# Optimization experiments

Hardware: AMD Instinct MI355X
Metric: run time of the kernel (lower is better)

The kernel has to match this reference:

```python
import jax, jax.numpy as jnp
import numpy as np

NUM_HEADS = 6


def setup_inputs() -> dict:
    key = jax.random.key(0)
    k1, k2, k3 = jax.random.split(key, 3)
    b_, n, c = 512, 256, 192
    nw = 64
    x = jax.random.normal(k1, (b_, n, c), dtype=jnp.float32)
    mask = jnp.zeros((nw, n, n), dtype=jnp.float32)  # 0 / -inf additive window mask
    W_qkv = jax.random.normal(k2, (3 * c, c), dtype=jnp.float32) * 0.02
    W_proj = jax.random.normal(k3, (c, c), dtype=jnp.float32) * 0.02
    b_proj = jnp.zeros((c,), dtype=jnp.float32)
    return {"x": x, "mask": mask, "W_qkv": W_qkv, "W_proj": W_proj, "b_proj": b_proj}


def reference(x, mask, W_qkv, W_proj, b_proj):
    b_, n, c = x.shape
    h = NUM_HEADS
    d = c // h
    scale = d ** (-0.5)
    # qkv projection (no bias): (b_, n, 3, h, d) -> (3, b_, h, n, d)
    qkv = (x @ W_qkv.T).reshape(b_, n, 3, h, d).transpose(2, 0, 3, 1, 4)
    q, k, v = qkv[0], qkv[1], qkv[2]
    q = q * scale
    attn = jnp.einsum('bhid,bhjd->bhij', q, k)  # (b_, h, n, n)
    nw = mask.shape[0]
    # add per-window mask bias: view as (B, nw, h, n, n) + (1, nw, 1, n, n)
    attn = attn.reshape(b_ // nw, nw, h, n, n) + mask[None, :, None, :, :]
    attn = attn.reshape(b_, h, n, n)
    attn = jax.nn.softmax(attn, axis=-1)
    out = jnp.einsum('bhij,bhjd->bhid', attn, v)  # (b_, h, n, d)
    out = out.transpose(0, 2, 1, 3).reshape(b_, n, c)
    return out @ W_proj.T + b_proj
```

## Files before the change

### kernel.cpp

```cpp
#include <hip/hip_runtime.h>
#include <hip/hip_bf16.h>
#include <stdint.h>

typedef short bf16x8 __attribute__((ext_vector_type(8)));
typedef float f32x4 __attribute__((ext_vector_type(4)));

#define B_   512
#define N_   256
#define C_   192
#define H_   6
#define D_   32
#define NW_  64

__device__ __forceinline__ uint16_t f2bf(float f) {
    uint32_t u = __builtin_bit_cast(uint32_t, f);
    u += 0x7FFFu + ((u >> 16) & 1u);
    return (uint16_t)(u >> 16);
}

__device__ __forceinline__ uint32_t pk_bf16(float a, float b) {
    float2 t; t.x = a; t.y = b;
    __hip_bfloat162 h = __float22bfloat162_rn(t);
    uint32_t u;
    __builtin_memcpy(&u, &h, 4);
    return u;
}

__device__ __forceinline__ bf16x8 ld_bf8(const uint16_t* p) {
    uint4 u = *reinterpret_cast<const uint4*>(p);
    return __builtin_bit_cast(bf16x8, u);
}

__global__ void prep_kernel(const float* __restrict__ mask,
                            const float* __restrict__ wqkv,
                            const float* __restrict__ wproj,
                            uint16_t* __restrict__ sel,
                            uint16_t* __restrict__ wqkv_bf,
                            uint16_t* __restrict__ wproj_bf,
                            unsigned* __restrict__ flag) {
    const int64_t NSEL = (int64_t)NW_ * N_ * N_;
    const int64_t NWQ  = 3 * C_ * C_;
    const int64_t NWP  = (int64_t)C_ * C_;
    int64_t i = (int64_t)blockIdx.x * blockDim.x + threadIdx.x;
    int64_t stride = (int64_t)gridDim.x * blockDim.x;
    bool nz = false;
    for (; i < NSEL + NWQ + NWP; i += stride) {
        if (i < NSEL) {
            float m = mask[i];
            nz |= (m != 0.0f);
            sel[i] = (m == 0.0f) ? 0xFFFFu : 0u;
        } else if (i < NSEL + NWQ) {
            int64_t j = i - NSEL;
            wqkv_bf[j] = f2bf(wqkv[j]);
        } else {
            int64_t j = i - NSEL - NWQ;
            wproj_bf[j] = f2bf(wproj[j]);
        }
    }
    if (flag && __any(nz) && ((threadIdx.x & 63) == 0))
        atomicOr(flag, 1u);
}

#define SA 200
#define SB 72
__global__ __launch_bounds__(512, 4)
void qkv_kernel(const float* __restrict__ x, const uint16_t* __restrict__ wq,
                uint16_t* __restrict__ qbuf, uint16_t* __restrict__ kbuf,
                uint16_t* __restrict__ vtbuf) {
    __shared__ __align__(16) uint16_t Alds[128 * SA];
    __shared__ __align__(16) uint16_t Blds[192 * SB];
    const int tid  = threadIdx.x;
    const int lane = tid & 63;
    const int wv   = tid >> 6;
    const int wrow = wv >> 2;
    const int wcol = wv & 3;
    const int quad = lane >> 4;
    const int l15  = lane & 15;
    const int m0   = blockIdx.x * 128;

#pragma unroll
    for (int p = 0; p < 12; p++) {
        int f = p * 512 + tid;
        int row = f / 48, c4 = f % 48;
        const float4 v = *reinterpret_cast<const float4*>(
            x + (int64_t)(m0 + row) * 192 + c4 * 4);
        uint2 d;
        d.x = pk_bf16(v.x, v.y);
        d.y = pk_bf16(v.z, v.w);
        *reinterpret_cast<uint2*>(&Alds[row * SA + c4 * 4]) = d;
    }

    const float scale = 0.17677669529663687f * 1.4426950408889634f;

    for (int cb = 0; cb < 3; cb++) {
        f32x4 acc[4][3];
#pragma unroll
        for (int i = 0; i < 4; i++)
#pragma unroll
            for (int j = 0; j < 3; j++) acc[i][j] = (f32x4)0.f;

        for (int k0 = 0; k0 < 192; k0 += 64) {
            __syncthreads();
#pragma unroll
            for (int p = 0; p < 3; p++) {
                int u = p * 512 + tid;
                int row = u >> 3, c8 = u & 7;
                uint4 w = *reinterpret_cast<const uint4*>(
                    wq + (int64_t)(cb * 192 + row) * 192 + k0 + c8 * 8);
                *reinterpret_cast<uint4*>(&Blds[row * SB + c8 * 8]) = w;
            }
            __syncthreads();
#pragma unroll
            for (int ks = 0; ks < 2; ks++) {
                bf16x8 xf[4], wf[3];
#pragma unroll
                for (int i = 0; i < 4; i++)
                    xf[i] = *reinterpret_cast<const bf16x8*>(
                        &Alds[(wrow * 64 + i * 16 + l15) * SA + k0 + ks * 32 + quad * 8]);
#pragma unroll
                for (int j = 0; j < 3; j++)
                    wf[j] = *reinterpret_cast<const bf16x8*>(
                        &Blds[(wcol * 48 + j * 16 + l15) * SB + ks * 32 + quad * 8]);
                if (cb < 2) {
#pragma unroll
                    for (int i = 0; i < 4; i++)
#pragma unroll
                        for (int j = 0; j < 3; j++)
                            acc[i][j] = __builtin_amdgcn_mfma_f32_16x16x32_bf16(
                                wf[j], xf[i], acc[i][j], 0, 0, 0);
                } else {
#pragma unroll
                    for (int i = 0; i < 4; i++)
#pragma unroll
                        for (int j = 0; j < 3; j++)
                            acc[i][j] = __builtin_amdgcn_mfma_f32_16x16x32_bf16(
                                xf[i], wf[j], acc[i][j], 0, 0, 0);
                }
            }
        }

        if (cb < 2) {
            uint16_t* dst = (cb == 0) ? qbuf : kbuf;
            const float sc = (cb == 0) ? scale : 1.0f;
#pragma unroll
            for (int i = 0; i < 4; i++) {
                int m = m0 + wrow * 64 + i * 16 + l15;
                int b = m >> 8, pos = m & 255;
#pragma unroll
                for (int j = 0; j < 3; j++) {
                    int cbase = wcol * 48 + j * 16 + quad * 4;
                    int h = cbase >> 5, d0 = cbase & 31;
                    int64_t bh = (int64_t)b * H_ + h;
                    uint2 s;
                    s.x = pk_bf16(acc[i][j][0] * sc, acc[i][j][1] * sc);
                    s.y = pk_bf16(acc[i][j][2] * sc, acc[i][j][3] * sc);
                    *reinterpret_cast<uint2*>(&dst[(bh * N_ + pos) * D_ + d0]) = s;
                }
            }
        } else {
#pragma unroll
            for (int i = 0; i < 4; i++) {
                int m = m0 + wrow * 64 + i * 16 + quad * 4;
                int b = m >> 8, pos0 = m & 255;
#pragma unroll
                for (int j = 0; j < 3; j++) {
                    int c = wcol * 48 + j * 16 + l15;
                    int h = c >> 5, d = c & 31;
                    int64_t bh = (int64_t)b * H_ + h;
                    uint2 s;
                    s.x = pk_bf16(acc[i][j][0], acc[i][j][1]);
                    s.y = pk_bf16(acc[i][j][2], acc[i][j][3]);
                    *reinterpret_cast<uint2*>(&vtbuf[(bh * D_ + d) * N_ + pos0]) = s;
                }
            }
        }
    }
}

__global__ __launch_bounds__(256, 3)
void attn_kernel(const uint16_t* __restrict__ qbuf, const uint16_t* __restrict__ kbuf,
                 const uint16_t* __restrict__ vtbuf, const uint16_t* __restrict__ sel,
                 const unsigned* __restrict__ flag,
                 uint16_t* __restrict__ aout) {
    __shared__ __align__(16) uint16_t Plds[4 * 2 * 32 * 40];
    const int bi = blockIdx.x;
    const int h  = bi % 6;
    const int r_ = bi / 6;
    const int ih = r_ & 1;
    const int g  = (r_ >> 1) & 7;
    const int w  = r_ >> 4;
    const int b  = g * 64 + w;
    const int tid  = threadIdx.x;
    const int lane = tid & 63;
    const int wv   = tid >> 6;
    const int quad = lane >> 4;
    const int l15  = lane & 15;
    const int i0   = ih * 128 + wv * 32;
    const bool hasmask = flag ? (*flag != 0u) : true;
    const int64_t bh = (int64_t)b * H_ + h;
    const uint16_t* qB = qbuf  + bh * N_ * D_;
    const uint16_t* kB = kbuf  + bh * N_ * D_;
    const uint16_t* vB = vtbuf + bh * D_ * N_;
    const uint16_t* sB = sel   + (int64_t)w * N_ * N_;
    uint16_t* Pw = &Plds[wv * 2 * 32 * 40];

    bf16x8 qf[2];
#pragma unroll
    for (int it = 0; it < 2; it++)
        qf[it] = ld_bf8(&qB[(i0 + it * 16 + l15) * D_ + quad * 8]);

    f32x4 oacc[2][2];
    f32x4 lacc[2];
#pragma unroll
    for (int mt = 0; mt < 2; mt++) {
        oacc[mt][0] = (f32x4)0.f; oacc[mt][1] = (f32x4)0.f; lacc[mt] = (f32x4)0.f;
    }
    bf16x8 ones;
#pragma unroll
    for (int e = 0; e < 8; e++) ones[e] = (short)0x3F80;

    bf16x8 kf[4];
#pragma unroll
    for (int jt = 0; jt < 4; jt++)
        kf[jt] = ld_bf8(&kB[(jt * 16 + l15) * D_ + quad * 8]);

    for (int jc = 0; jc < 4; jc++) {
        const int j0 = jc * 64;

        bf16x8 kfn[4];
        if (jc < 3) {
#pragma unroll
            for (int jt = 0; jt < 4; jt++)
                kfn[jt] = ld_bf8(&kB[(j0 + 64 + jt * 16 + l15) * D_ + quad * 8]);
        }

        bf16x8 vf[2][2];
#pragma unroll
        for (int hf = 0; hf < 2; hf++)
#pragma unroll
            for (int nt = 0; nt < 2; nt++)
                vf[hf][nt] = ld_bf8(&vB[(nt * 16 + l15) * N_ + j0 + hf * 32 + quad * 8]);

        uint4 sv[2][2];
        if (hasmask) {
#pragma unroll
            for (int hf = 0; hf < 2; hf++)
#pragma unroll
                for (int mt = 0; mt < 2; mt++)
                    sv[hf][mt] = *reinterpret_cast<const uint4*>(
                        &sB[(int64_t)(i0 + mt * 16 + l15) * N_ + j0 + hf * 32 + quad * 8]);
        } else {
#pragma unroll
            for (int hf = 0; hf < 2; hf++)
#pragma unroll
                for (int mt = 0; mt < 2; mt++)
                    sv[hf][mt] = make_uint4(~0u, ~0u, ~0u, ~0u);
        }

#pragma unroll
        for (int hf = 0; hf < 2; hf++) {
            f32x4 sacc[2][2];
#pragma unroll
            for (int jt2 = 0; jt2 < 2; jt2++)
#pragma unroll
                for (int it = 0; it < 2; it++) sacc[jt2][it] = (f32x4)0.f;
            __builtin_amdgcn_s_setprio(1);
#pragma unroll
            for (int jt2 = 0; jt2 < 2; jt2++)
#pragma unroll
                for (int it = 0; it < 2; it++)
                    sacc[jt2][it] = __builtin_amdgcn_mfma_f32_16x16x32_bf16(
                        kf[hf * 2 + jt2], qf[it], sacc[jt2][it], 0, 0, 0);
            __builtin_amdgcn_s_setprio(0);

            uint16_t* Ph = Pw + hf * (32 * 40);
#pragma unroll
            for (int it = 0; it < 2; it++)
#pragma unroll
                for (int jt2 = 0; jt2 < 2; jt2++) {
                    f32x4 s = sacc[jt2][it];
                    uint2 d;
                    d.x = pk_bf16(__builtin_amdgcn_exp2f(s[0]),
                                  __builtin_amdgcn_exp2f(s[1]));
                    d.y = pk_bf16(__builtin_amdgcn_exp2f(s[2]),
                                  __builtin_amdgcn_exp2f(s[3]));
                    *reinterpret_cast<uint2*>(
                        &Ph[(it * 16 + l15) * 40 + jt2 * 16 + quad * 4]) = d;
                }

#pragma unroll
            for (int mt = 0; mt < 2; mt++) {
                uint4 p = *reinterpret_cast<const uint4*>(
                    &Ph[(mt * 16 + l15) * 40 + quad * 8]);
                p.x &= sv[hf][mt].x; p.y &= sv[hf][mt].y;
                p.z &= sv[hf][mt].z; p.w &= sv[hf][mt].w;
                bf16x8 pa = __builtin_bit_cast(bf16x8, p);
                __builtin_amdgcn_s_setprio(1);
                oacc[mt][0] = __builtin_amdgcn_mfma_f32_16x16x32_bf16(pa, vf[hf][0], oacc[mt][0], 0, 0, 0);
                oacc[mt][1] = __builtin_amdgcn_mfma_f32_16x16x32_bf16(pa, vf[hf][1], oacc[mt][1], 0, 0, 0);
                lacc[mt]    = __builtin_amdgcn_mfma_f32_16x16x32_bf16(pa, ones,      lacc[mt],    0, 0, 0);
                __builtin_amdgcn_s_setprio(0);
            }
        }

        if (jc < 3) {
#pragma unroll
            for (int jt = 0; jt < 4; jt++) kf[jt] = kfn[jt];
        }
    }

#pragma unroll
    for (int mt = 0; mt < 2; mt++)
#pragma unroll
        for (int r4 = 0; r4 < 4; r4++) {
            float inv = 1.0f / lacc[mt][r4];
            int i = i0 + mt * 16 + quad * 4 + r4;
#pragma unroll
            for (int nt = 0; nt < 2; nt++) {
                float v = oacc[mt][nt][r4] * inv;
                aout[((int64_t)b * N_ + i) * C_ + h * 32 + nt * 16 + l15] = f2bf(v);
            }
        }
}

__global__ __launch_bounds__(512, 2)
void proj_kernel(const uint16_t* __restrict__ a, const uint16_t* __restrict__ wp,
                 const float* __restrict__ bias, float* __restrict__ out) {
    __shared__ __align__(16) uint16_t Alds[128 * 72];
    __shared__ __align__(16) uint16_t Blds[192 * 72];
    const int tid  = threadIdx.x;
    const int lane = tid & 63;
    const int wv   = tid >> 6;
    const int wm   = wv >> 2;
    const int wn   = wv & 3;
    const int quad = lane >> 4;
    const int l15  = lane & 15;
    const int m0   = blockIdx.x * 128;

    f32x4 acc[4][3];
#pragma unroll
    for (int x = 0; x < 4; x++)
#pragma unroll
        for (int y = 0; y < 3; y++) acc[x][y] = (f32x4)0.f;

    for (int k0 = 0; k0 < 192; k0 += 64) {
        __syncthreads();
#pragma unroll
        for (int p = 0; p < 2; p++) {
            int u = tid + p * 512;
            int row = u >> 3, c8 = u & 7;
            uint4 v = *reinterpret_cast<const uint4*>(
                a + (int64_t)(m0 + row) * 192 + k0 + c8 * 8);
            *reinterpret_cast<uint4*>(&Alds[row * 72 + c8 * 8]) = v;
        }
#pragma unroll
        for (int p = 0; p < 3; p++) {
            int u = tid + p * 512;
            int row = u >> 3, c8 = u & 7;
            uint4 v = *reinterpret_cast<const uint4*>(
                wp + (int64_t)row * 192 + k0 + c8 * 8);
            *reinterpret_cast<uint4*>(&Blds[row * 72 + c8 * 8]) = v;
        }
        __syncthreads();
#pragma unroll
        for (int ks = 0; ks < 2; ks++) {
            bf16x8 af[4], bfr[3];
#pragma unroll
            for (int mt = 0; mt < 4; mt++)
                af[mt] = *reinterpret_cast<const bf16x8*>(
                    &Alds[(wm * 64 + mt * 16 + l15) * 72 + ks * 32 + quad * 8]);
#pragma unroll
            for (int nt = 0; nt < 3; nt++)
                bfr[nt] = *reinterpret_cast<const bf16x8*>(
                    &Blds[(wn * 48 + nt * 16 + l15) * 72 + ks * 32 + quad * 8]);
#pragma unroll
            for (int mt = 0; mt < 4; mt++)
#pragma unroll
                for (int nt = 0; nt < 3; nt++)
                    acc[mt][nt] = __builtin_amdgcn_mfma_f32_16x16x32_bf16(
                        af[mt], bfr[nt], acc[mt][nt], 0, 0, 0);
        }
    }
    float bv[3];
#pragma unroll
    for (int nt = 0; nt < 3; nt++) bv[nt] = bias[wn * 48 + nt * 16 + l15];
#pragma unroll
    for (int mt = 0; mt < 4; mt++)
#pragma unroll
        for (int r = 0; r < 4; r++) {
            int m = m0 + wm * 64 + mt * 16 + quad * 4 + r;
#pragma unroll
            for (int nt = 0; nt < 3; nt++) {
                int col = wn * 48 + nt * 16 + l15;
                out[(int64_t)m * 192 + col] = acc[mt][nt][r] + bv[nt];
            }
        }
}

extern "C" void kernel_launch(void* const* d_in, const int* in_sizes, int n_in,
                              void* d_out, int out_size, void* d_ws, size_t ws_size,
                              hipStream_t stream) {
    const float* x     = (const float*)d_in[0];
    const float* mask  = (const float*)d_in[1];
    const float* wqkv  = (const float*)d_in[2];
    const float* wproj = (const float*)d_in[3];
    const float* bproj = (const float*)d_in[4];
    float* out = (float*)d_out;

    uint16_t* qbuf = (uint16_t*)d_out;
    uint16_t* kbuf = qbuf + 25165824;
    char* ws = (char*)d_ws;
    uint16_t* vtbuf = (uint16_t*)(ws);
    uint16_t* aout  = (uint16_t*)(ws + 50331648);
    uint16_t* sel   = (uint16_t*)(ws + 100663296);
    uint16_t* wq_bf = (uint16_t*)(ws + 109051904);
    uint16_t* wp_bf = (uint16_t*)(ws + 109273088);
    unsigned* flag  = nullptr;
    if (ws_size >= 109346816 + 4)
        flag = (unsigned*)(ws + 109346816);

    if (flag) hipMemsetAsync(flag, 0, 4, stream);
    prep_kernel<<<4096, 256, 0, stream>>>(mask, wqkv, wproj, sel, wq_bf, wp_bf, flag);
    qkv_kernel<<<1024, 512, 0, stream>>>(x, wq_bf, qbuf, kbuf, vtbuf);
    attn_kernel<<<6144, 256, 0, stream>>>(qbuf, kbuf, vtbuf, sel, flag, aout);
    proj_kernel<<<1024, 512, 0, stream>>>(aout, wp_bf, bproj, out);
}
```

Before: 325.5 us.

## Load GEMM weight fragments directly from global memory, drop LDS staging and barriers

Result: slower. 442.0 us (+35.8%).

```diff
diff --git a/kernel.cpp b/kernel.cpp
--- a/kernel.cpp
+++ b/kernel.cpp
@@ -62,13 +62,11 @@
 }
 
 #define SA 200
-#define SB 72
 __global__ __launch_bounds__(512, 4)
 void qkv_kernel(const float* __restrict__ x, const uint16_t* __restrict__ wq,
                 uint16_t* __restrict__ qbuf, uint16_t* __restrict__ kbuf,
                 uint16_t* __restrict__ vtbuf) {
     __shared__ __align__(16) uint16_t Alds[128 * SA];
-    __shared__ __align__(16) uint16_t Blds[192 * SB];
     const int tid  = threadIdx.x;
     const int lane = tid & 63;
     const int wv   = tid >> 6;
@@ -89,6 +87,7 @@
         d.y = pk_bf16(v.z, v.w);
         *reinterpret_cast<uint2*>(&Alds[row * SA + c4 * 4]) = d;
     }
+    __syncthreads();
 
     const float scale = 0.17677669529663687f * 1.4426950408889634f;
 
@@ -99,43 +98,46 @@
 #pragma unroll
             for (int j = 0; j < 3; j++) acc[i][j] = (f32x4)0.f;
 
-        for (int k0 = 0; k0 < 192; k0 += 64) {
-            __syncthreads();
-#pragma unroll
-            for (int p = 0; p < 3; p++) {
-                int u = p * 512 + tid;
-                int row = u >> 3, c8 = u & 7;
-                uint4 w = *reinterpret_cast<const uint4*>(
-                    wq + (int64_t)(cb * 192 + row) * 192 + k0 + c8 * 8);
-                *reinterpret_cast<uint4*>(&Blds[row * SB + c8 * 8]) = w;
-            }
-            __syncthreads();
-#pragma unroll
-            for (int ks = 0; ks < 2; ks++) {
-                bf16x8 xf[4], wf[3];
+        const uint16_t* wB = wq + ((int64_t)cb * 192 + wcol * 48 + l15) * 192;
+
+        bf16x8 wf[3], wfn[3];
+#pragma unroll
+        for (int j = 0; j < 3; j++)
+            wf[j] = ld_bf8(wB + j * 16 * 192 + quad * 8);
+
+#pragma unroll
+        for (int kk = 0; kk < 6; kk++) {
+            const int kb = kk * 32;
+            if (kk < 5) {
+#pragma unroll
+                for (int j = 0; j < 3; j++)
+                    wfn[j] = ld_bf8(wB + j * 16 * 192 + kb + 32 + quad * 8);
+            }
+            bf16x8 xf[4];
+#pragma unroll
+            for (int i = 0; i < 4; i++)
+                xf[i] = *reinterpret_cast<const bf16x8*>(
+                    &Alds[(wrow * 64 + i * 16 + l15) * SA + kb + quad * 8]);
+            __builtin_amdgcn_s_setprio(1);
+            if (cb < 2) {
 #pragma unroll
                 for (int i = 0; i < 4; i++)
-                    xf[i] = *reinterpret_cast<const bf16x8*>(
-                        &Alds[(wrow * 64 + i * 16 + l15) * SA + k0 + ks * 32 + quad * 8]);
-#pragma unroll
-                for (int j = 0; j < 3; j++)
-                    wf[j] = *reinterpret_cast<const bf16x8*>(
-                        &Blds[(wcol * 48 + j * 16 + l15) * SB + ks * 32 + quad * 8]);
-                if (cb < 2) {
-#pragma unroll
-                    for (int i = 0; i < 4; i++)
-#pragma unroll
-                        for (int j = 0; j < 3; j++)
-                            acc[i][j] = __builtin_amdgcn_mfma_f32_16x16x32_bf16(
-                                wf[j], xf[i], acc[i][j], 0, 0, 0);
-                } else {
-#pragma unroll
-                    for (int i = 0; i < 4; i++)
-#pragma unroll
-                        for (int j = 0; j < 3; j++)
-                            acc[i][j] = __builtin_amdgcn_mfma_f32_16x16x32_bf16(
-                                xf[i], wf[j], acc[i][j], 0, 0, 0);
-                }
+#pragma unroll
+                    for (int j = 0; j < 3; j++)
+                        acc[i][j] = __builtin_amdgcn_mfma_f32_16x16x32_bf16(
+                            wf[j], xf[i], acc[i][j], 0, 0, 0);
+            } else {
+#pragma unroll
+                for (int i = 0; i < 4; i++)
+#pragma unroll
+                    for (int j = 0; j < 3; j++)
+                        acc[i][j] = __builtin_amdgcn_mfma_f32_16x16x32_bf16(
+                            xf[i], wf[j], acc[i][j], 0, 0, 0);
+            }
+            __builtin_amdgcn_s_setprio(0);
+            if (kk < 5) {
+#pragma unroll
+                for (int j = 0; j < 3; j++) wf[j] = wfn[j];
             }
         }
 
@@ -323,11 +325,10 @@
         }
 }
 
-__global__ __launch_bounds__(512, 2)
+__global__ __launch_bounds__(512, 4)
 void proj_kernel(const uint16_t* __restrict__ a, const uint16_t* __restrict__ wp,
                  const float* __restrict__ bias, float* __restrict__ out) {
-    __shared__ __align__(16) uint16_t Alds[128 * 72];
-    __shared__ __align__(16) uint16_t Blds[192 * 72];
+    __shared__ __align__(16) uint16_t Alds[128 * SA];
     const int tid  = threadIdx.x;
     const int lane = tid & 63;
     const int wv   = tid >> 6;
@@ -337,50 +338,55 @@
     const int l15  = lane & 15;
     const int m0   = blockIdx.x * 128;
 
+#pragma unroll
+    for (int p = 0; p < 6; p++) {
+        int u = p * 512 + tid;
+        int row = u / 24, c8 = u % 24;
+        uint4 v = *reinterpret_cast<const uint4*>(
+            a + (int64_t)(m0 + row) * 192 + c8 * 8);
+        *reinterpret_cast<uint4*>(&Alds[row * SA + c8 * 8]) = v;
+    }
+    __syncthreads();
+
     f32x4 acc[4][3];
 #pragma unroll
     for (int x = 0; x < 4; x++)
 #pragma unroll
         for (int y = 0; y < 3; y++) acc[x][y] = (f32x4)0.f;
 
-    for (int k0 = 0; k0 < 192; k0 += 64) {
-        __syncthreads();
-#pragma unroll
-        for (int p = 0; p < 2; p++) {
-            int u = tid + p * 512;
-            int row = u >> 3, c8 = u & 7;
-            uint4 v = *reinterpret_cast<const uint4*>(
-                a + (int64_t)(m0 + row) * 192 + k0 + c8 * 8);
-            *reinterpret_cast<uint4*>(&Alds[row * 72 + c8 * 8]) = v;
-        }
-#pragma unroll
-        for (int p = 0; p < 3; p++) {
-            int u = tid + p * 512;
-            int row = u >> 3, c8 = u & 7;
-            uint4 v = *reinterpret_cast<const uint4*>(
-                wp + (int64_t)row * 192 + k0 + c8 * 8);
-            *reinterpret_cast<uint4*>(&Blds[row * 72 + c8 * 8]) = v;
-        }
-        __syncthreads();
-#pragma unroll
-        for (int ks = 0; ks < 2; ks++) {
-            bf16x8 af[4], bfr[3];
-#pragma unroll
-            for (int mt = 0; mt < 4; mt++)
-                af[mt] = *reinterpret_cast<const bf16x8*>(
-                    &Alds[(wm * 64 + mt * 16 + l15) * 72 + ks * 32 + quad * 8]);
+    const uint16_t* wB = wp + (int64_t)(wn * 48 + l15) * 192;
+    bf16x8 bfr[3], bfn[3];
+#pragma unroll
+    for (int nt = 0; nt < 3; nt++)
+        bfr[nt] = ld_bf8(wB + nt * 16 * 192 + quad * 8);
+
+#pragma unroll
+    for (int kk = 0; kk < 6; kk++) {
+        const int kb = kk * 32;
+        if (kk < 5) {
 #pragma unroll
             for (int nt = 0; nt < 3; nt++)
-                bfr[nt] = *reinterpret_cast<const bf16x8*>(
-                    &Blds[(wn * 48 + nt * 16 + l15) * 72 + ks * 32 + quad * 8]);
-#pragma unroll
-            for (int mt = 0; mt < 4; mt++)
-#pragma unroll
-                for (int nt = 0; nt < 3; nt++)
-                    acc[mt][nt] = __builtin_amdgcn_mfma_f32_16x16x32_bf16(
-                        af[mt], bfr[nt], acc[mt][nt], 0, 0, 0);
-        }
-    }
+                bfn[nt] = ld_bf8(wB + nt * 16 * 192 + kb + 32 + quad * 8);
+        }
+        bf16x8 af[4];
+#pragma unroll
+        for (int mt = 0; mt < 4; mt++)
+            af[mt] = *reinterpret_cast<const bf16x8*>(
+                &Alds[(wm * 64 + mt * 16 + l15) * SA + kb + quad * 8]);
+        __builtin_amdgcn_s_setprio(1);
+#pragma unroll
+        for (int mt = 0; mt < 4; mt++)
+#pragma unroll
+            for (int nt = 0; nt < 3; nt++)
+                acc[mt][nt] = __builtin_amdgcn_mfma_f32_16x16x32_bf16(
+                    af[mt], bfr[nt], acc[mt][nt], 0, 0, 0);
+        __builtin_amdgcn_s_setprio(0);
+        if (kk < 5) {
+#pragma unroll
+            for (int nt = 0; nt < 3; nt++) bfr[nt] = bfn[nt];
+        }
+    }
+
     float bv[3];
 #pragma unroll
     for (int nt = 0; nt < 3; nt++) bv[nt] = bias[wn * 48 + nt * 16 + l15];
```
